# Kernel optimization log

Hardware: AMD Instinct MI355X
Metric: run time of the kernel (lower is better)

Reference implementation:

```python
import math
import jax, jax.numpy as jnp
import numpy as np

HEADS = 8
DIM_HEAD = 64
MAX_POS_EMB = 512


def setup_inputs() -> dict:
    key = jax.random.key(0)
    ks = jax.random.split(key, 6)
    dim = 512
    inner = HEADS * DIM_HEAD  # 512
    x = jax.random.normal(ks[0], (16, 3900, dim), jnp.float32)
    wq = jax.random.normal(ks[1], (dim, inner), jnp.float32) * 0.02
    wkv = jax.random.normal(ks[2], (dim, 2 * inner), jnp.float32) * 0.02
    wout_w = jax.random.normal(ks[3], (inner, dim), jnp.float32) * 0.02
    wout_b = jax.random.normal(ks[4], (dim,), jnp.float32) * 0.02
    rel_pos_table = jax.random.normal(ks[5], (2 * MAX_POS_EMB + 1, DIM_HEAD), jnp.float32) * 0.02
    return {"x": x, "wq": wq, "wkv": wkv, "wout_w": wout_w, "wout_b": wout_b,
            "rel_pos_table": rel_pos_table, "context_size": 200}


def reference(x, wq, wkv, wout_w, wout_b, rel_pos_table, context_size):
    bs, n, d = x.shape
    h, dh = HEADS, DIM_HEAD
    c = context_size
    scale = dh ** -0.5
    nb = math.ceil(n / c)
    nr = n % c
    if nr > 0:
        x = jnp.pad(x, ((0, 0), (0, c - nr), (0, 0)))  # [bs, nb*c, d]
    np_tok = nb * c
    q = x @ wq                     # [bs, np, inner]
    kv = x @ wkv                   # [bs, np, 2*inner]
    k, v = jnp.split(kv, 2, axis=-1)
    # [bs, nb, c, h, dh] -> [bs, nb, h, c, dh]
    def to_heads(t):
        return t.reshape(bs, nb, c, h, dh).transpose(0, 1, 3, 2, 4)
    q, k, v = to_heads(q), to_heads(k), to_heads(v)
    dots = jnp.einsum('bmhid,bmhjd->bmhij', q, k) * scale  # [bs, nb, h, c, c]
    # relative position bias (Transformer-XL style within chunk)
    seq = jnp.arange(c)
    dist = jnp.clip(seq[:, None] - seq[None, :], -c, c) + MAX_POS_EMB  # [c, c]
    rel = rel_pos_table[dist]  # [c, c, dh]
    pos_attn = jnp.einsum('bmhcd,crd->bmhcr', q, rel) * scale
    dots = dots + pos_attn
    if nr > 0:
        # last chunk: mask everything except the valid top-left nr x nr block
        mask = jnp.ones((c, c), dtype=bool).at[:nr, :nr].set(False)
        mask_value = -jnp.finfo(dots.dtype).max
        dots = dots.at[:, -1].set(jnp.where(mask, mask_value, dots[:, -1]))
    attn = jax.nn.softmax(dots, axis=-1)
    out = jnp.einsum('bmhij,bmhjd->bmhid', attn, v)  # [bs, nb, h, c, dh]
    out = out.transpose(0, 1, 3, 2, 4).reshape(bs, np_tok, h * dh)
    out = out[:, :n, :] @ wout_w + wout_b  # dropout is identity at eval
    return out
```

## Files before the change

### kernel.cpp

```cpp
#include <hip/hip_runtime.h>
#include <hip/hip_bf16.h>
#include <cstdint>
#include <cstddef>

#define BS 16
#define SEQ 3900
#define DIM 512
#define NHEAD 8
#define DH 64
#define CHUNK 200
#define NB 20
#define NR 100
#define NP 4000
#define MAXPOS 512
#define MD 62400

typedef __attribute__((ext_vector_type(8))) short bf16x8;
typedef __attribute__((ext_vector_type(8))) unsigned short u16x8;
typedef __attribute__((ext_vector_type(4))) float f32x4;
#define MFMA_BF16 __builtin_amdgcn_mfma_f32_16x16x32_bf16

static __device__ __forceinline__ float bf2f(unsigned short u) {
  union { unsigned int i; float f; } v; v.i = ((unsigned int)u) << 16; return v.f;
}
static __device__ __forceinline__ unsigned short f2bf(float f) {
  unsigned int x = __float_as_uint(f);
  unsigned int lsb = (x >> 16) & 1u;
  x += 0x7fffu + lsb;
  return (unsigned short)(x >> 16);
}

static __device__ __forceinline__ void gload16(const void* g, void* l) {
  auto gp = reinterpret_cast<const __attribute__((address_space(1))) unsigned int*>(
      reinterpret_cast<uintptr_t>(g));
  auto lp = reinterpret_cast<__attribute__((address_space(3))) unsigned int*>(
      reinterpret_cast<uintptr_t>(l));
  __builtin_amdgcn_global_load_lds(gp, lp, 16, 0, 0);
}

static __device__ __forceinline__ const unsigned short* wt_row(
    const unsigned short* base, int n) {
  unsigned ch = (unsigned)n / 100u;
  unsigned rr = (unsigned)n - ch * 100u;
  return base + (size_t)ch * (NP * DIM) + (size_t)SEQ * DIM + (size_t)rr * DIM;
}

__global__ __launch_bounds__(256) void prep_table(
    const float* __restrict__ table, unsigned short* __restrict__ Tb)
{
  int idx = (blockIdx.x * 256 + threadIdx.x) * 4;
  if (idx < 416 * 64) {
    float4 f = *reinterpret_cast<const float4*>(table + (size_t)305 * 64 + idx);
    ushort4 o;
    o.x = f2bf(f.x); o.y = f2bf(f.y); o.z = f2bf(f.z); o.w = f2bf(f.w);
    *reinterpret_cast<ushort4*>(Tb + idx) = o;
  }
}

__global__ __launch_bounds__(256) void wtrans(
    const float* __restrict__ W, int ldn, int n_off,
    unsigned short* __restrict__ base)
{
  __shared__ float ts[64][65];
  const int tid = threadIdx.x;
  const int n0 = blockIdx.x * 64;
  const int k0 = blockIdx.y * 64;
  {
    int kl = tid >> 4;
    int nl = (tid & 15) * 4;
#pragma unroll
    for (int p = 0; p < 4; ++p) {
      float4 f = *reinterpret_cast<const float4*>(
          W + (size_t)(k0 + kl + p * 16) * ldn + n0 + nl);
      ts[kl + p * 16][nl + 0] = f.x;
      ts[kl + p * 16][nl + 1] = f.y;
      ts[kl + p * 16][nl + 2] = f.z;
      ts[kl + p * 16][nl + 3] = f.w;
    }
  }
  __syncthreads();
  {
    int nl = tid >> 2;
    int kof = (tid & 3) * 16;
    int n = n0 + nl + n_off;
    unsigned ch = (unsigned)n / 100u;
    unsigned rr = (unsigned)n - ch * 100u;
    unsigned short* dst = base + (size_t)ch * (NP * DIM) + (size_t)SEQ * DIM
                          + (size_t)rr * DIM + k0 + kof;
    u16x8 o0, o1;
#pragma unroll
    for (int i = 0; i < 8; ++i) o0[i] = f2bf(ts[kof + i][nl]);
#pragma unroll
    for (int i = 0; i < 8; ++i) o1[i] = f2bf(ts[kof + 8 + i][nl]);
    *reinterpret_cast<u16x8*>(dst) = o0;
    *reinterpret_cast<u16x8*>(dst + 8) = o1;
  }
}

__global__ __launch_bounds__(256) void cast_x(
    const float* __restrict__ x, unsigned short* __restrict__ xb)
{
  const size_t total = (size_t)MD * DIM;
  size_t i = ((size_t)blockIdx.x * 256 + threadIdx.x) * 8;
  const size_t stride = (size_t)gridDim.x * 256 * 8;
  for (; i < total; i += stride) {
    float4 f0 = *reinterpret_cast<const float4*>(x + i);
    float4 f1 = *reinterpret_cast<const float4*>(x + i + 4);
    u16x8 o;
    o[0] = f2bf(f0.x); o[1] = f2bf(f0.y); o[2] = f2bf(f0.z); o[3] = f2bf(f0.w);
    o[4] = f2bf(f1.x); o[5] = f2bf(f1.y); o[6] = f2bf(f1.z); o[7] = f2bf(f1.w);
    *reinterpret_cast<u16x8*>(xb + i) = o;
  }
}

__global__ __launch_bounds__(256) void gemm_qkv(
    const unsigned short* __restrict__ xb, const unsigned short* __restrict__ WtBase,
    unsigned short* __restrict__ Qb, unsigned short* __restrict__ Kb,
    unsigned short* __restrict__ Vb)
{
  __shared__ unsigned short As[2][8 * 512];
  __shared__ unsigned short Bs[2][8 * 512];

  int bid = blockIdx.x;
  bid = (bid & 7) * 732 + (bid >> 3);
  const int bm = bid / 12, bn = bid % 12;
  const int m0 = bm * 128, n0 = bn * 128;
  const int tid = threadIdx.x;
  const int wv = tid >> 6, ln = tid & 63;
  const int wr = wv >> 1, wc = wv & 1;
  const int lr = ln & 15, lg = ln >> 4;

  const int sl = ln & 15, sk = (ln >> 4) * 8;
  const int q0 = wv * 2, q1 = q0 + 1;
  int ar0 = m0 + (q0 >> 2) * 64 + (q0 & 3) * 16 + sl; if (ar0 >= MD) ar0 = MD - 1;
  int ar1 = m0 + (q1 >> 2) * 64 + (q1 & 3) * 16 + sl; if (ar1 >= MD) ar1 = MD - 1;
  const unsigned short* aS0 = xb + (size_t)ar0 * DIM + sk;
  const unsigned short* aS1 = xb + (size_t)ar1 * DIM + sk;
  const unsigned short* bS0 = wt_row(WtBase, n0 + (q0 >> 2) * 64 + (q0 & 3) * 16 + sl) + sk;
  const unsigned short* bS1 = wt_row(WtBase, n0 + (q1 >> 2) * 64 + (q1 & 3) * 16 + sl) + sk;

  f32x4 acc[4][4];
#pragma unroll
  for (int i = 0; i < 4; ++i)
#pragma unroll
    for (int j = 0; j < 4; ++j) acc[i][j] = (f32x4){0.f, 0.f, 0.f, 0.f};

#define STG_QKV(buf, koff)                          \
  gload16(aS0 + (koff), &As[buf][q0 * 512]);        \
  gload16(aS1 + (koff), &As[buf][q1 * 512]);        \
  gload16(bS0 + (koff), &Bs[buf][q0 * 512]);        \
  gload16(bS1 + (koff), &Bs[buf][q1 * 512]);

  STG_QKV(0, 0)
  __syncthreads();

  int p = 0;
  for (int s = 0; s < 16; ++s) {
    if (s < 15) { STG_QKV(p ^ 1, (s + 1) * 32) }
    const unsigned short* asp = As[p];
    const unsigned short* bsp = Bs[p];
    bf16x8 af[4], bfr[4];
#pragma unroll
    for (int mt = 0; mt < 4; ++mt)
      af[mt] = *reinterpret_cast<const bf16x8*>(asp + (wr * 4 + mt) * 512 + ln * 8);
#pragma unroll
    for (int nt = 0; nt < 4; ++nt)
      bfr[nt] = *reinterpret_cast<const bf16x8*>(bsp + (wc * 4 + nt) * 512 + ln * 8);
#pragma unroll
    for (int mt = 0; mt < 4; ++mt)
#pragma unroll
      for (int nt = 0; nt < 4; ++nt)
        acc[mt][nt] = MFMA_BF16(af[mt], bfr[nt], acc[mt][nt], 0, 0, 0);
    __syncthreads();
    p ^= 1;
  }

  unsigned short* dst; int nbase;
  if (n0 < 512)       { dst = Qb; nbase = 0; }
  else if (n0 < 1024) { dst = Kb; nbase = 512; }
  else                { dst = Vb; nbase = 1024; }
  const int colg0 = n0 + wc * 64 - nbase;
#pragma unroll
  for (int mt = 0; mt < 4; ++mt) {
#pragma unroll
    for (int e = 0; e < 4; ++e) {
      unsigned rd = m0 + wr * 64 + mt * 16 + lg * 4 + e;
      if (rd < MD) {
        unsigned bb = rd / 3900u;
        unsigned tt = rd - bb * 3900u;
        size_t rowoff = ((size_t)bb * NP + tt) * DIM;
#pragma unroll
        for (int nt = 0; nt < 4; ++nt)
          dst[rowoff + colg0 + nt * 16 + lr] = f2bf(acc[mt][nt][e]);
      }
    }
  }
}

__global__ __launch_bounds__(256) void gemm_out(
    const unsigned short* __restrict__ Ob, const unsigned short* __restrict__ WoBase,
    const float* __restrict__ bias, float* __restrict__ out)
{
  __shared__ unsigned short As[2][8 * 512];
  __shared__ unsigned short Bs[2][8 * 512];

  int bid = blockIdx.x;
  bid = (bid & 7) * 244 + (bid >> 3);
  const int bm = bid / 4, bn = bid % 4;
  const int m0 = bm * 128, n0 = bn * 128;
  const int tid = threadIdx.x;
  const int wv = tid >> 6, ln = tid & 63;
  const int wr = wv >> 1, wc = wv & 1;
  const int lr = ln & 15, lg = ln >> 4;

  const int sl = ln & 15, sk = (ln >> 4) * 8;
  const int q0 = wv * 2, q1 = q0 + 1;
  unsigned ar0 = m0 + (q0 >> 2) * 64 + (q0 & 3) * 16 + sl; if (ar0 >= MD) ar0 = MD - 1;
  unsigned ar1 = m0 + (q1 >> 2) * 64 + (q1 & 3) * 16 + sl; if (ar1 >= MD) ar1 = MD - 1;
  unsigned b0b = ar0 / 3900u, t0 = ar0 - b0b * 3900u;
  unsigned b1b = ar1 / 3900u, t1 = ar1 - b1b * 3900u;
  const unsigned short* aS0 = Ob + ((size_t)b0b * NP + t0) * DIM + sk;
  const unsigned short* aS1 = Ob + ((size_t)b1b * NP + t1) * DIM + sk;
  const unsigned short* bS0 = wt_row(WoBase, n0 + (q0 >> 2) * 64 + (q0 & 3) * 16 + sl) + sk;
  const unsigned short* bS1 = wt_row(WoBase, n0 + (q1 >> 2) * 64 + (q1 & 3) * 16 + sl) + sk;

  f32x4 acc[4][4];
#pragma unroll
  for (int i = 0; i < 4; ++i)
#pragma unroll
    for (int j = 0; j < 4; ++j) acc[i][j] = (f32x4){0.f, 0.f, 0.f, 0.f};

#define STG_OUT(buf, koff)                          \
  gload16(aS0 + (koff), &As[buf][q0 * 512]);        \
  gload16(aS1 + (koff), &As[buf][q1 * 512]);        \
  gload16(bS0 + (koff), &Bs[buf][q0 * 512]);        \
  gload16(bS1 + (koff), &Bs[buf][q1 * 512]);

  STG_OUT(0, 0)
  __syncthreads();

  int p = 0;
  for (int s = 0; s < 16; ++s) {
    if (s < 15) { STG_OUT(p ^ 1, (s + 1) * 32) }
    const unsigned short* asp = As[p];
    const unsigned short* bsp = Bs[p];
    bf16x8 af[4], bfr[4];
#pragma unroll
    for (int mt = 0; mt < 4; ++mt)
      af[mt] = *reinterpret_cast<const bf16x8*>(asp + (wr * 4 + mt) * 512 + ln * 8);
#pragma unroll
    for (int nt = 0; nt < 4; ++nt)
      bfr[nt] = *reinterpret_cast<const bf16x8*>(bsp + (wc * 4 + nt) * 512 + ln * 8);
#pragma unroll
    for (int mt = 0; mt < 4; ++mt)
#pragma unroll
      for (int nt = 0; nt < 4; ++nt)
        acc[mt][nt] = MFMA_BF16(af[mt], bfr[nt], acc[mt][nt], 0, 0, 0);
    __syncthreads();
    p ^= 1;
  }

  float bv[4];
#pragma unroll
  for (int nt = 0; nt < 4; ++nt) bv[nt] = bias[n0 + wc * 64 + nt * 16 + lr];
#pragma unroll
  for (int mt = 0; mt < 4; ++mt) {
#pragma unroll
    for (int e = 0; e < 4; ++e) {
      unsigned rd = m0 + wr * 64 + mt * 16 + lg * 4 + e;
      if (rd < MD) {
#pragma unroll
        for (int nt = 0; nt < 4; ++nt)
          out[(size_t)rd * DIM + n0 + wc * 64 + nt * 16 + lr] = acc[mt][nt][e] + bv[nt];
      }
    }
  }
}

#define KS_U16 12800
#define VT_U16 13568
#define PQ_STR 228
#define PQ_U16 (16*PQ_STR)
#define ATTN_LDS_B ((KS_U16 + VT_U16 + 4*PQ_U16) * 2)

__global__ __launch_bounds__(256) void attn_mfma(
    const unsigned short* __restrict__ Qb, const unsigned short* __restrict__ Kb,
    const unsigned short* __restrict__ Vb, const unsigned short* __restrict__ Tb,
    unsigned short* __restrict__ Ob)
{
  extern __shared__ unsigned short smem[];
  unsigned short* Ks = smem;
  unsigned short* Vt = smem + KS_U16;

  const int tid = threadIdx.x;
  const int bid = blockIdx.x;
  const int h  = bid & 7;
  const int bm = bid >> 3;
  const int m  = bm % NB;
  const int b  = bm / NB;
  const size_t rowbase = (size_t)b * NP + (size_t)m * CHUNK;
  const int lim = (m == NB - 1) ? NR : CHUNK;

  for (int c = tid; c < CHUNK * 8; c += 256) {
    int j = c >> 3, k0 = (c & 7) * 8;
    uint4 kv = *reinterpret_cast<const uint4*>(Kb + (rowbase + j) * DIM + h * DH + k0);
    int byte = (j * 128 + k0 * 2) ^ ((j & 7) << 4);
    *reinterpret_cast<uint4*>(reinterpret_cast<char*>(Ks) + byte) = kv;
    uint4 vv4 = *reinterpret_cast<const uint4*>(Vb + (rowbase + j) * DIM + h * DH + k0);
    const unsigned short* vs = reinterpret_cast<const unsigned short*>(&vv4);
#pragma unroll
    for (int e = 0; e < 8; ++e)
      Vt[(k0 + e) * 212 + j] = vs[e];
  }
  __syncthreads();

  const int wv = tid >> 6, ln = tid & 63;
  const int lr = ln & 15, lg = ln >> 4;
  unsigned short* pq = smem + KS_U16 + VT_U16 + wv * PQ_U16;

  const int nMt = (lim + 15) >> 4;
  for (int mt = wv; mt < nMt; mt += 4) {
    const int i0 = mt << 4;

    const unsigned short* qp = Qb + (rowbase + i0 + lr) * DIM + h * DH + lg * 8;
    bf16x8 qa0 = *reinterpret_cast<const bf16x8*>(qp);
    bf16x8 qa1 = *reinterpret_cast<const bf16x8*>(qp + 32);

#pragma unroll
    for (int ct = 0; ct < 14; ++ct) {
      const unsigned short* tp = Tb + (size_t)(i0 + ct * 16 + lr) * 64 + lg * 8;
      bf16x8 tb0 = *reinterpret_cast<const bf16x8*>(tp);
      bf16x8 tb1 = *reinterpret_cast<const bf16x8*>(tp + 32);
      f32x4 acc = {0.f, 0.f, 0.f, 0.f};
      acc = MFMA_BF16(qa0, tb0, acc, 0, 0, 0);
      acc = MFMA_BF16(qa1, tb1, acc, 0, 0, 0);
#pragma unroll
      for (int e = 0; e < 4; ++e)
        pq[(lg * 4 + e) * PQ_STR + ct * 16 + lr] = f2bf(acc[e]);
    }

    f32x4 s[13];
#pragma unroll
    for (int nt = 0; nt < 13; ++nt) {
      int row = nt * 16 + lr;
      int b0 = (row * 128 + lg * 16) ^ ((row & 7) << 4);
      int b1 = (row * 128 + 64 + lg * 16) ^ ((row & 7) << 4);
      bf16x8 k0 = *reinterpret_cast<const bf16x8*>(reinterpret_cast<char*>(Ks) + b0);
      bf16x8 k1 = *reinterpret_cast<const bf16x8*>(reinterpret_cast<char*>(Ks) + b1);
      f32x4 acc = {0.f, 0.f, 0.f, 0.f};
      acc = MFMA_BF16(qa0, k0, acc, 0, 0, 0);
      acc = MFMA_BF16(qa1, k1, acc, 0, 0, 0);
      s[nt] = acc;
    }

#pragma unroll
    for (int nt = 0; nt < 13; ++nt) {
      int j = nt * 16 + lr;
#pragma unroll
      for (int e = 0; e < 4; ++e) {
        int r = lg * 4 + e;
        float pos = bf2f(pq[r * PQ_STR + (r - j + 207)]);
        float v = (s[nt][e] + pos) * 0.125f;
        s[nt][e] = (j < lim) ? v : -INFINITY;
      }
    }

    float sum[4];
#pragma unroll
    for (int e = 0; e < 4; ++e) {
      float mv = s[0][e];
#pragma unroll
      for (int nt = 1; nt < 13; ++nt) mv = fmaxf(mv, s[nt][e]);
      mv = fmaxf(mv, __shfl_xor(mv, 1));
      mv = fmaxf(mv, __shfl_xor(mv, 2));
      mv = fmaxf(mv, __shfl_xor(mv, 4));
      mv = fmaxf(mv, __shfl_xor(mv, 8));
      float sv = 0.f;
#pragma unroll
      for (int nt = 0; nt < 13; ++nt) {
        float p = __expf(s[nt][e] - mv);
        s[nt][e] = p;
        sv += p;
      }
      sv += __shfl_xor(sv, 1);
      sv += __shfl_xor(sv, 2);
      sv += __shfl_xor(sv, 4);
      sv += __shfl_xor(sv, 8);
      sum[e] = sv;
    }

#pragma unroll
    for (int nt = 0; nt < 13; ++nt)
#pragma unroll
      for (int e = 0; e < 4; ++e)
        pq[(lg * 4 + e) * PQ_STR + nt * 16 + lr] = f2bf(s[nt][e]);

    f32x4 o[4];
#pragma unroll
    for (int nt = 0; nt < 4; ++nt) o[nt] = (f32x4){0.f, 0.f, 0.f, 0.f};
    const ushort4 zz = {0, 0, 0, 0};
#pragma unroll
    for (int ks = 0; ks < 7; ++ks) {
      union __align__(16) { struct { ushort4 lo, hi; } u; bf16x8 v; } pa;
      if (ks < 6 || lg < 2) {
        const char* pap = reinterpret_cast<const char*>(pq) + lr * (PQ_STR * 2) + ks * 64 + lg * 16;
        pa.u.lo = *reinterpret_cast<const ushort4*>(pap);
        pa.u.hi = *reinterpret_cast<const ushort4*>(pap + 8);
      } else {
        pa.u.lo = zz; pa.u.hi = zz;
      }
#pragma unroll
      for (int nt = 0; nt < 4; ++nt) {
        union __align__(16) { struct { ushort4 lo, hi; } u; bf16x8 v; } vb;
        if (ks < 6 || lg == 0) {
          const char* vbp = reinterpret_cast<const char*>(Vt) + (nt * 16 + lr) * 424 + ks * 64 + lg * 16;
          vb.u.lo = *reinterpret_cast<const ushort4*>(vbp);
          vb.u.hi = *reinterpret_cast<const ushort4*>(vbp + 8);
        } else {
          vb.u.lo = zz; vb.u.hi = zz;
        }
        o[nt] = MFMA_BF16(pa.v, vb.v, o[nt], 0, 0, 0);
      }
    }

#pragma unroll
    for (int nt = 0; nt < 4; ++nt)
#pragma unroll
      for (int e = 0; e < 4; ++e) {
        int i = i0 + lg * 4 + e;
        if (i < lim) {
          float val = o[nt][e] / sum[e];
          Ob[(rowbase + i) * DIM + h * DH + nt * 16 + lr] = f2bf(val);
        }
      }
  }
}

extern "C" void kernel_launch(void* const* d_in, const int* in_sizes, int n_in,
                              void* d_out, int out_size, void* d_ws, size_t ws_size,
                              hipStream_t stream) {
  const float* x   = (const float*)d_in[0];
  const float* wq  = (const float*)d_in[1];
  const float* wkv = (const float*)d_in[2];
  const float* wo  = (const float*)d_in[3];
  const float* wb  = (const float*)d_in[4];
  const float* tbl = (const float*)d_in[5];
  float* out = (float*)d_out;

  const size_t elems = (size_t)BS * NP * DIM;
  unsigned short* Qb = (unsigned short*)d_ws;
  unsigned short* Kb = Qb + elems;
  unsigned short* Vb = Kb + elems;
  unsigned short* Ob = Qb;
  unsigned short* Tb = Kb + (size_t)SEQ * DIM;
  unsigned short* xb = (unsigned short*)d_out;

  hipFuncSetAttribute(reinterpret_cast<const void*>(attn_mfma),
                      hipFuncAttributeMaxDynamicSharedMemorySize, ATTN_LDS_B);

  dim3 blk(256);
  prep_table<<<dim3(26), blk, 0, stream>>>(tbl, Tb);
  wtrans<<<dim3(8, 8),  blk, 0, stream>>>(wq,  512,  0,   Qb);
  wtrans<<<dim3(16, 8), blk, 0, stream>>>(wkv, 1024, 512, Qb);
  wtrans<<<dim3(8, 8),  blk, 0, stream>>>(wo,  512,  0,   Vb);
  cast_x<<<dim3(2048), blk, 0, stream>>>(x, xb);
  gemm_qkv<<<dim3(5856), blk, 0, stream>>>(xb, Qb, Qb, Kb, Vb);
  attn_mfma<<<dim3(BS * NB * NHEAD), blk, ATTN_LDS_B, stream>>>(Qb, Kb, Vb, Tb, Ob);
  gemm_out<<<dim3(1952), blk, 0, stream>>>(Ob, Vb, wb, out);
}
```

Before: 508.2 us.

## Fold softmax scale and log2e into Wq, drop max pass, use exp2

Folds the 1/sqrt(dh) scale and log2(e) into the Wq weight conversion so attention scores come out already in the base-2 domain. The softmax then uses exp2f with no row-max subtraction, removing the max reduction and its shuffles, and replaces the final division with a reciprocal multiply. The position-bias buffer is stored as packed hardware bf16 conversions in a swizzled layout to ease LDS access. Skipping the max subtraction risks overflow if scores grow large, and the bf16 rounding of Q now happens after scaling.

```diff
diff --git a/kernel.cpp b/kernel.cpp
--- a/kernel.cpp
+++ b/kernel.cpp
@@ -29,6 +29,14 @@
   x += 0x7fffu + lsb;
   return (unsigned short)(x >> 16);
 }
+static __device__ __forceinline__ unsigned int cvtpk(float lo, float hi) {
+  unsigned int r;
+  asm("v_cvt_pk_bf16_f32 %0, %1, %2" : "=v"(r) : "v"(lo), "v"(hi));
+  return r;
+}
+static __device__ __forceinline__ unsigned short cvt1(float v) {
+  return (unsigned short)cvtpk(v, v);
+}
 
 static __device__ __forceinline__ void gload16(const void* g, void* l) {
   auto gp = reinterpret_cast<const __attribute__((address_space(1))) unsigned int*>(
@@ -58,7 +66,7 @@
 }
 
 __global__ __launch_bounds__(256) void wtrans(
-    const float* __restrict__ W, int ldn, int n_off,
+    const float* __restrict__ W, int ldn, int n_off, float scale,
     unsigned short* __restrict__ base)
 {
   __shared__ float ts[64][65];
@@ -89,9 +97,9 @@
                           + (size_t)rr * DIM + k0 + kof;
     u16x8 o0, o1;
 #pragma unroll
-    for (int i = 0; i < 8; ++i) o0[i] = f2bf(ts[kof + i][nl]);
-#pragma unroll
-    for (int i = 0; i < 8; ++i) o1[i] = f2bf(ts[kof + 8 + i][nl]);
+    for (int i = 0; i < 8; ++i) o0[i] = f2bf(ts[kof + i][nl] * scale);
+#pragma unroll
+    for (int i = 0; i < 8; ++i) o1[i] = f2bf(ts[kof + 8 + i][nl] * scale);
     *reinterpret_cast<u16x8*>(dst) = o0;
     *reinterpret_cast<u16x8*>(dst + 8) = o1;
   }
@@ -317,6 +325,7 @@
   const int wv = tid >> 6, ln = tid & 63;
   const int lr = ln & 15, lg = ln >> 4;
   unsigned short* pq = smem + KS_U16 + VT_U16 + wv * PQ_U16;
+  unsigned int* qtP = reinterpret_cast<unsigned int*>(pq);
 
   const int nMt = (lim + 15) >> 4;
   for (int mt = wv; mt < nMt; mt += 4) {
@@ -326,18 +335,24 @@
     bf16x8 qa0 = *reinterpret_cast<const bf16x8*>(qp);
     bf16x8 qa1 = *reinterpret_cast<const bf16x8*>(qp + 32);
 
-#pragma unroll
-    for (int ct = 0; ct < 14; ++ct) {
-      const unsigned short* tp = Tb + (size_t)(i0 + ct * 16 + lr) * 64 + lg * 8;
-      bf16x8 tb0 = *reinterpret_cast<const bf16x8*>(tp);
-      bf16x8 tb1 = *reinterpret_cast<const bf16x8*>(tp + 32);
-      f32x4 acc = {0.f, 0.f, 0.f, 0.f};
-      acc = MFMA_BF16(qa0, tb0, acc, 0, 0, 0);
-      acc = MFMA_BF16(qa1, tb1, acc, 0, 0, 0);
-#pragma unroll
-      for (int e = 0; e < 4; ++e)
-        pq[(lg * 4 + e) * PQ_STR + ct * 16 + lr] = f2bf(acc[e]);
-    }
+    {
+      const int c = 0;
+#pragma unroll
+      for (int ct = 0; ct < 14; ++ct) {
+        const unsigned short* tp = Tb + (size_t)(i0 + ct * 16 + lr) * 64 + lg * 8;
+        bf16x8 tb0 = *reinterpret_cast<const bf16x8*>(tp);
+        bf16x8 tb1 = *reinterpret_cast<const bf16x8*>(tp + 32);
+        f32x4 acc = {0.f, 0.f, 0.f, 0.f};
+        acc = MFMA_BF16(qa0, tb0, acc, 0, 0, 0);
+        acc = MFMA_BF16(qa1, tb1, acc, 0, 0, 0);
+        int cc = ct * 16 + lr;
+        int xr = (cc >> 2) & 7;
+        qtP[cc * 8 + ((lg * 2 + 0) ^ xr)] = cvtpk(acc[0], acc[1]);
+        qtP[cc * 8 + ((lg * 2 + 1) ^ xr)] = cvtpk(acc[2], acc[3]);
+      }
+      (void)c;
+    }
+    asm volatile("" ::: "memory");
 
     f32x4 s[13];
 #pragma unroll
@@ -353,47 +368,38 @@
       s[nt] = acc;
     }
 
+    float sv[4] = {0.f, 0.f, 0.f, 0.f};
+    const unsigned short* qt16 = reinterpret_cast<const unsigned short*>(qtP);
 #pragma unroll
     for (int nt = 0; nt < 13; ++nt) {
       int j = nt * 16 + lr;
 #pragma unroll
       for (int e = 0; e < 4; ++e) {
         int r = lg * 4 + e;
-        float pos = bf2f(pq[r * PQ_STR + (r - j + 207)]);
-        float v = (s[nt][e] + pos) * 0.125f;
-        s[nt][e] = (j < lim) ? v : -INFINITY;
-      }
-    }
-
-    float sum[4];
+        int cc = r - j + 207;
+        unsigned short pu = qt16[(cc * 8 + ((r >> 1) ^ ((cc >> 2) & 7))) * 2 + (r & 1)];
+        float t = s[nt][e] + bf2f(pu);
+        float p = (j < lim) ? exp2f(t) : 0.f;
+        s[nt][e] = p;
+        sv[e] += p;
+      }
+    }
 #pragma unroll
     for (int e = 0; e < 4; ++e) {
-      float mv = s[0][e];
-#pragma unroll
-      for (int nt = 1; nt < 13; ++nt) mv = fmaxf(mv, s[nt][e]);
-      mv = fmaxf(mv, __shfl_xor(mv, 1));
-      mv = fmaxf(mv, __shfl_xor(mv, 2));
-      mv = fmaxf(mv, __shfl_xor(mv, 4));
-      mv = fmaxf(mv, __shfl_xor(mv, 8));
-      float sv = 0.f;
-#pragma unroll
-      for (int nt = 0; nt < 13; ++nt) {
-        float p = __expf(s[nt][e] - mv);
-        s[nt][e] = p;
-        sv += p;
-      }
-      sv += __shfl_xor(sv, 1);
-      sv += __shfl_xor(sv, 2);
-      sv += __shfl_xor(sv, 4);
-      sv += __shfl_xor(sv, 8);
-      sum[e] = sv;
-    }
+      float x = sv[e];
+      x += __shfl_xor(x, 1);
+      x += __shfl_xor(x, 2);
+      x += __shfl_xor(x, 4);
+      x += __shfl_xor(x, 8);
+      sv[e] = __builtin_amdgcn_rcpf(x);
+    }
+    asm volatile("" ::: "memory");
 
 #pragma unroll
     for (int nt = 0; nt < 13; ++nt)
 #pragma unroll
       for (int e = 0; e < 4; ++e)
-        pq[(lg * 4 + e) * PQ_STR + nt * 16 + lr] = f2bf(s[nt][e]);
+        pq[(lg * 4 + e) * PQ_STR + nt * 16 + lr] = cvt1(s[nt][e]);
 
     f32x4 o[4];
 #pragma unroll
@@ -429,8 +435,7 @@
       for (int e = 0; e < 4; ++e) {
         int i = i0 + lg * 4 + e;
         if (i < lim) {
-          float val = o[nt][e] / sum[e];
-          Ob[(rowbase + i) * DIM + h * DH + nt * 16 + lr] = f2bf(val);
+          Ob[(rowbase + i) * DIM + h * DH + nt * 16 + lr] = cvt1(o[nt][e] * sv[e]);
         }
       }
   }
@@ -458,11 +463,12 @@
   hipFuncSetAttribute(reinterpret_cast<const void*>(attn_mfma),
                       hipFuncAttributeMaxDynamicSharedMemorySize, ATTN_LDS_B);
 
+  const float qscale = 0.125f * 1.44269504088896f;
   dim3 blk(256);
   prep_table<<<dim3(26), blk, 0, stream>>>(tbl, Tb);
-  wtrans<<<dim3(8, 8),  blk, 0, stream>>>(wq,  512,  0,   Qb);
-  wtrans<<<dim3(16, 8), blk, 0, stream>>>(wkv, 1024, 512, Qb);
-  wtrans<<<dim3(8, 8),  blk, 0, stream>>>(wo,  512,  0,   Vb);
+  wtrans<<<dim3(8, 8),  blk, 0, stream>>>(wq,  512,  0,   qscale, Qb);
+  wtrans<<<dim3(16, 8), blk, 0, stream>>>(wkv, 1024, 512, 1.0f,   Qb);
+  wtrans<<<dim3(8, 8),  blk, 0, stream>>>(wo,  512,  0,   1.0f,   Vb);
   cast_x<<<dim3(2048), blk, 0, stream>>>(x, xb);
   gemm_qkv<<<dim3(5856), blk, 0, stream>>>(xb, Qb, Qb, Kb, Vb);
   attn_mfma<<<dim3(BS * NB * NHEAD), blk, ATTN_LDS_B, stream>>>(Qb, Kb, Vb, Tb, Ob);
```

After: 610.8 us. 1.2x slower.
